# Optimization experiments

Hardware: AMD Instinct MI355X
Metric: run time of the kernel (lower is better)

The kernel has to match this reference:

```python
import jax, jax.numpy as jnp
from jax import lax
import numpy as np

LRELU_SLOPE = 0.01  # PyTorch LeakyReLU default
BETA = 0.25


def lrelu(x):
    return jnp.where(x >= 0, x, LRELU_SLOPE * x)


def conv2d(x, w, b, stride, pad):
    # x: [B,C,H,W], w: [Cout,Cin,k,k] (torch OIHW)
    y = lax.conv_general_dilated(x, w, (stride, stride), ((pad, pad), (pad, pad)),
                                 dimension_numbers=('NCHW', 'OIHW', 'NCHW'))
    return y + b[None, :, None, None]


def conv_transpose2d(x, w, b, stride, out_pad):
    # w: torch ConvTranspose2d weight [Cin,Cout,k,k]; implement as dilated conv
    # with spatially flipped kernel. out = (i-1)*stride + k + out_pad.
    wf = jnp.flip(w, (2, 3)).transpose(1, 0, 2, 3)  # -> [Cout,Cin,k,k]
    k = w.shape[2]
    pad = ((k - 1, k - 1 + out_pad), (k - 1, k - 1 + out_pad))
    y = lax.conv_general_dilated(x, wf, (1, 1), pad, lhs_dilation=(stride, stride),
                                 dimension_numbers=('NCHW', 'OIHW', 'NCHW'))
    return y + b[None, :, None, None]


def setup_inputs() -> dict:
    key = jax.random.key(0)
    ks = jax.random.split(key, 16)
    s = 0.05
    inp = {
        'x':   jax.random.normal(ks[0], (64, 1, 256, 256), jnp.float32),
        'ew1': jax.random.normal(ks[1], (8, 1, 4, 4), jnp.float32) * s,
        'eb1': jnp.zeros((8,), jnp.float32),
        'ew2': jax.random.normal(ks[2], (16, 8, 4, 4), jnp.float32) * s,
        'eb2': jnp.zeros((16,), jnp.float32),
        'ew3': jax.random.normal(ks[3], (32, 16, 4, 4), jnp.float32) * s,
        'eb3': jnp.zeros((32,), jnp.float32),
        'ew4': jax.random.normal(ks[4], (32, 32, 3, 3), jnp.float32) * s,
        'eb4': jnp.zeros((32,), jnp.float32),
        'ew5': jax.random.normal(ks[5], (64, 32, 1, 1), jnp.float32) * s,
        'eb5': jnp.zeros((64,), jnp.float32),
        'dw1': jax.random.normal(ks[6], (32, 64, 3, 3), jnp.float32) * s,
        'db1': jnp.zeros((32,), jnp.float32),
        'dw2': jax.random.normal(ks[7], (32, 16, 4, 4), jnp.float32) * s,
        'db2': jnp.zeros((16,), jnp.float32),
        'dw3': jax.random.normal(ks[8], (16, 8, 4, 4), jnp.float32) * s,
        'db3': jnp.zeros((8,), jnp.float32),
        'dw4': jax.random.normal(ks[9], (8, 1, 4, 4), jnp.float32) * s,
        'db4': jnp.zeros((1,), jnp.float32),
        # nn.init.uniform_(-1/K, 1/K) with K=512
        'codebook': jax.random.uniform(ks[10], (512, 64), jnp.float32,
                                       minval=-1.0 / 512, maxval=1.0 / 512),
    }
    return inp


def vqvae_forward(x, ew1, eb1, ew2, eb2, ew3, eb3, ew4, eb4, ew5, eb5,
                  dw1, db1, dw2, db2, dw3, db3, dw4, db4, codebook):
    # ---- encoder ----
    h = lrelu(conv2d(x, ew1, eb1, 2, 0))   # [B,8,127,127]
    h = lrelu(conv2d(h, ew2, eb2, 2, 0))   # [B,16,62,62]
    h = lrelu(conv2d(h, ew3, eb3, 2, 0))   # [B,32,30,30]
    h = lrelu(conv2d(h, ew4, eb4, 1, 1))   # [B,32,30,30]
    h = lrelu(conv2d(h, ew5, eb5, 1, 0))   # [B,64,30,30]
    # ---- vector quantizer ----
    lat = h.transpose(0, 2, 3, 1)                      # [B,h,w,D]
    D = lat.shape[-1]
    flat = lat.reshape(-1, D)                          # [N,D]
    # squared euclidean distances via expansion (same argmin as torch.norm)
    d2 = (jnp.sum(flat * flat, axis=1, keepdims=True)
          - 2.0 * flat @ codebook.T
          + jnp.sum(codebook * codebook, axis=1))      # [N,K]
    idx = jnp.argmin(d2, axis=1)                       # [N]
    q = codebook[idx].reshape(lat.shape)               # [B,h,w,D]
    commitment = jnp.mean((lax.stop_gradient(q) - lat) ** 2)
    embedding = jnp.mean((q - lax.stop_gradient(lat)) ** 2)
    vq_loss = commitment * BETA + embedding
    q_st = lat + lax.stop_gradient(q - lat)            # straight-through
    z = q_st.transpose(0, 3, 1, 2)                     # [B,D,h,w]
    # ---- decoder ----
    h = lrelu(conv2d(z, dw1, db1, 1, 1))               # [B,32,30,30]
    h = lrelu(conv_transpose2d(h, dw2, db2, 2, 1))     # [B,16,63,63]
    h = lrelu(conv_transpose2d(h, dw3, db3, 2, 1))     # [B,8,131,131]
    recons = jnp.tanh(conv_transpose2d(h, dw4, db4, 2, 0))  # [B,1,264,264]
    return recons, vq_loss


def reference(x, ew1, eb1, ew2, eb2, ew3, eb3, ew4, eb4, ew5, eb5,
              dw1, db1, dw2, db2, dw3, db3, dw4, db4, codebook):
    return vqvae_forward(x, ew1, eb1, ew2, eb2, ew3, eb3, ew4, eb4, ew5, eb5,
                         dw1, db1, dw2, db2, dw3, db3, dw4, db4, codebook)
```

## Files before the change

### kernel.cpp

```cpp
#include <hip/hip_runtime.h>
#include <hip/hip_bf16.h>
#include <math.h>

#define LRELU 0.01f

template<int NW>
__device__ __forceinline__ void ldw(const float* p, float* w) {
    if constexpr (NW % 4 == 0) {
#pragma unroll
        for (int u = 0; u < NW / 4; u++) {
            float4 v = *(const float4*)(p + 4 * u);
            w[4*u] = v.x; w[4*u+1] = v.y; w[4*u+2] = v.z; w[4*u+3] = v.w;
        }
    } else {
#pragma unroll
        for (int c = 0; c < NW; c++) w[c] = p[c];
    }
}

__device__ __forceinline__ void wfwd(const float* s, float* d, int CIN, int COUT,
                                     int KK, int i) {
    int co = i / (CIN * KK); int r = i - co * CIN * KK;
    int ci = r / KK; int t = r - ci * KK;
    d[(ci * KK + t) * COUT + co] = s[i];
}
__device__ __forceinline__ void wtr(const float* s, float* d, int CIN, int COUT,
                                    int KK, int i) {
    int ci = i / (COUT * KK); int r = i - ci * COUT * KK;
    int co = r / KK; int t = r - co * KK;
    d[(t * CIN + ci) * COUT + co] = s[i];
}
__global__ __launch_bounds__(256)
void prep_k(const float* e1, const float* e2, const float* e3, const float* e4,
            const float* e5, const float* d1, const float* d2, const float* d3,
            const float* d4, float* w, const float* cbp, float* hcbn,
            unsigned long long* keys, float* loss, int* idxm, int N) {
    int i = blockIdx.x * 256 + threadIdx.x;
    if      (i < 128)   wfwd(e1, w + 0,     1,  8, 16, i);
    else if (i < 2176)  wfwd(e2, w + 128,   8, 16, 16, i - 128);
    else if (i < 10368) wfwd(e3, w + 2176, 16, 32, 16, i - 2176);
    else if (i < 19584) wfwd(e4, w + 10368, 32, 32, 9, i - 10368);
    else if (i < 21632) wfwd(e5, w + 19584, 32, 64, 1, i - 19584);
    else if (i < 40064) wfwd(d1, w + 21632, 64, 32, 9, i - 21632);
    else if (i < 48256) wtr (d2, w + 40064, 32, 16, 16, i - 40064);
    else if (i < 50304) wtr (d3, w + 48256, 16,  8, 16, i - 48256);
    else if (i < 50432) wtr (d4, w + 50304,  8,  1, 16, i - 50304);
    else if (i < 50944) {
        int k = i - 50432;
        const float* c = cbp + k * 64;
        float s = 0.f;
#pragma unroll
        for (int d = 0; d < 64; d++) s = fmaf(c[d], c[d], s);
        hcbn[k] = 0.5f * s;
    } else if (i < 50944 + N) {
        keys[i - 50944] = 0xFFFFFFFFFFFFFFFFull;
    } else if (i == 50944 + N) {
        loss[0] = 0.f;
    } else if (i < 50945 + N + 64 * 124) {
        int j = i - (50945 + N);
        int b2 = j / 124, s = j - b2 * 124;
        int r, c;
        if (s < 32)      { r = 0;  c = s; }
        else if (s < 64) { r = 31; c = s - 32; }
        else { int u = s - 64; r = 1 + (u >> 1); c = (u & 1) * 31; }
        idxm[b2 * 1024 + r * 32 + c] = 512;
    }
}

__global__ __launch_bounds__(256)
void ubuild_k(const float* __restrict__ w, const float* __restrict__ cb,
              float* __restrict__ U) {
    int g = blockIdx.x * 256 + threadIdx.x;
    if (g >= 513 * 288) return;
    if (g >= 512 * 288) { U[g] = 0.f; return; }
    int k = g / 288, rem = g - k * 288;
    const float* cr = cb + k * 64;
    float s = 0.f;
#pragma unroll 4
    for (int ci = 0; ci < 64; ci++)
        s = fmaf(w[ci * 288 + rem], cr[ci], s);
    U[g] = s;
}

template<int CIN, int COUT, int CO_BLK, int HIN, int ISTR, int HOUT, int WOUT,
         int OPLANE, int OSTR, int OPAD, int CB, int RB, int ZCONV, int ZF_CH>
__global__ __launch_bounds__(256)
void convs2_k(const float* __restrict__ in, const float* __restrict__ wt,
              const float* __restrict__ bias, float* __restrict__ out) {
    const int b = blockIdx.x, cog = blockIdx.y, tid = threadIdx.x;
    if (ZF_CH > 0 && (int)blockIdx.z >= ZCONV) {
        if (cog != 0) return;
        int i = ((int)blockIdx.z - ZCONV) * 256 + tid;
        if (i >= ZF_CH * 124) return;
        int ch = i / 124, s = i - ch * 124;
        int r, c;
        if (s < 32)      { r = 0;  c = s; }
        else if (s < 64) { r = 31; c = s - 32; }
        else { int u = s - 64; r = 1 + (u >> 1); c = (u & 1) * 31; }
        out[(size_t)(b * ZF_CH + ch) * 1024 + r * 32 + c] = 0.f;
        return;
    }
    __shared__ __align__(16) float lw[CIN * 16 * CO_BLK];
    for (int i = tid; i < CIN * 16 * CO_BLK; i += 256) {
        int row = i / CO_BLK, c = i - row * CO_BLK;
        lw[i] = wt[row * COUT + cog * CO_BLK + c];
    }
    __syncthreads();

    const int tz = blockIdx.z;
    const int cbi = tz / RB, rb = tz - cbi * RB;
    const int tx = tid & 15, ty = tid >> 4;
    const int ow0 = (cbi * 16 + tx) * 2;
    const int oh  = rb * 16 + ty;
    if (oh >= HOUT || ow0 >= WOUT) return;
    const bool p1v = (ow0 + 1) < WOUT;

    float acc[CO_BLK][2];
#pragma unroll
    for (int c = 0; c < CO_BLK; c++) {
        float bv = bias[cog * CO_BLK + c];
        acc[c][0] = bv; acc[c][1] = bv;
    }
    const float* inb = in + ((size_t)(b * CIN) * HIN + oh * 2) * ISTR + ow0 * 2;
#pragma unroll 2
    for (int ci = 0; ci < CIN; ci++) {
        const float* r = inb + (size_t)ci * HIN * ISTR;
        float4 a4[4]; float2 b2[4];
#pragma unroll
        for (int kh = 0; kh < 4; kh++) {
            a4[kh] = *(const float4*)(r + kh * ISTR);
            b2[kh] = p1v ? *(const float2*)(r + kh * ISTR + 4) : make_float2(0.f, 0.f);
        }
        const float* wr = lw + ci * 16 * CO_BLK;
#pragma unroll
        for (int kh = 0; kh < 4; kh++) {
            float x0[4] = {a4[kh].x, a4[kh].y, a4[kh].z, a4[kh].w};
            float x1[4] = {a4[kh].z, a4[kh].w, b2[kh].x, b2[kh].y};
#pragma unroll
            for (int kw = 0; kw < 4; kw++) {
                float wv[CO_BLK];
                ldw<CO_BLK>(wr + (kh * 4 + kw) * CO_BLK, wv);
#pragma unroll
                for (int c = 0; c < CO_BLK; c++) {
                    acc[c][0] = fmaf(x0[kw], wv[c], acc[c][0]);
                    acc[c][1] = fmaf(x1[kw], wv[c], acc[c][1]);
                }
            }
        }
    }
    float* ob = out + (size_t)(b * COUT + cog * CO_BLK) * OPLANE
                    + (oh + OPAD) * OSTR + ow0 + OPAD;
#pragma unroll
    for (int c = 0; c < CO_BLK; c++) {
        float v0 = acc[c][0]; v0 = (v0 >= 0.f) ? v0 : LRELU * v0;
        ob[(size_t)c * OPLANE] = v0;
        if (p1v) {
            float v1 = acc[c][1]; v1 = (v1 >= 0.f) ? v1 : LRELU * v1;
            ob[(size_t)c * OPLANE + 1] = v1;
        }
    }
}

template<int CIN, int COUT, int CO_BLK, int OPLANE, int OSTR, int OPADH, int OPADV,
         bool ZSIDE>
__global__ __launch_bounds__(256)
void conv3_k(const float* __restrict__ in, const float* __restrict__ wt,
             const float* __restrict__ bias, float* __restrict__ out) {
    const int b = blockIdx.x, cog = blockIdx.y, tid = threadIdx.x;
    __shared__ __align__(16) float lw[CIN * 9 * CO_BLK];
    for (int i = tid; i < CIN * 9 * CO_BLK; i += 256) {
        int row = i / CO_BLK, c = i - row * CO_BLK;
        lw[i] = wt[row * COUT + cog * CO_BLK + c];
    }
    __syncthreads();

    const int rb = blockIdx.z;
    const int tx = tid & 15, ty = tid >> 4;
    const int r = rb * 16 + ty;
    if (r >= 30) return;
    const int ow0 = tx * 2;
    if (tx == 15) {
        if (ZSIDE) {
#pragma unroll
            for (int c = 0; c < CO_BLK; c++) {
                float* base = out + (size_t)(b * COUT + cog * CO_BLK + c) * OPLANE
                                  + (r + OPADV) * OSTR;
                base[0] = 0.f; base[31] = 0.f; base[32] = 0.f;
            }
        }
        return;
    }
    float acc[CO_BLK][2];
#pragma unroll
    for (int c = 0; c < CO_BLK; c++) {
        float bv = bias[cog * CO_BLK + c];
        acc[c][0] = bv; acc[c][1] = bv;
    }
    const float* inb = in + ((size_t)(b * CIN) * 32 + r) * 32 + ow0;
#pragma unroll 2
    for (int ci = 0; ci < CIN; ci++) {
        const float* rr = inb + (size_t)ci * 1024;
        float2 A[3], Bv[3];
#pragma unroll
        for (int kh = 0; kh < 3; kh++) {
            A[kh]  = *(const float2*)(rr + kh * 32);
            Bv[kh] = *(const float2*)(rr + kh * 32 + 2);
        }
        const float* wr = lw + ci * 9 * CO_BLK;
#pragma unroll
        for (int kh = 0; kh < 3; kh++) {
            float x0[3] = {A[kh].x, A[kh].y, Bv[kh].x};
            float x1[3] = {A[kh].y, Bv[kh].x, Bv[kh].y};
#pragma unroll
            for (int kw = 0; kw < 3; kw++) {
                float wv[CO_BLK];
                ldw<CO_BLK>(wr + (kh * 3 + kw) * CO_BLK, wv);
#pragma unroll
                for (int c = 0; c < CO_BLK; c++) {
                    acc[c][0] = fmaf(x0[kw], wv[c], acc[c][0]);
                    acc[c][1] = fmaf(x1[kw], wv[c], acc[c][1]);
                }
            }
        }
    }
    float* ob = out + (size_t)(b * COUT + cog * CO_BLK) * OPLANE
                    + (r + OPADV) * OSTR + ow0 + OPADH;
#pragma unroll
    for (int c = 0; c < CO_BLK; c++) {
        float v0 = acc[c][0]; v0 = (v0 >= 0.f) ? v0 : LRELU * v0;
        float v1 = acc[c][1]; v1 = (v1 >= 0.f) ? v1 : LRELU * v1;
        ob[(size_t)c * OPLANE] = v0;
        ob[(size_t)c * OPLANE + 1] = v1;
    }
}

template<int CIN, int COUT, int CO_BLK>
__global__ __launch_bounds__(256)
void conv1_k(const float* __restrict__ in, const float* __restrict__ wt,
             const float* __restrict__ bias, float* __restrict__ out) {
    __shared__ __align__(16) float lw[CIN * CO_BLK];
    const int b = blockIdx.x, cog = blockIdx.y;
    for (int i = threadIdx.x; i < CIN * CO_BLK; i += 256) {
        int row = i / CO_BLK, c = i - row * CO_BLK;
        lw[i] = wt[row * COUT + cog * CO_BLK + c];
    }
    __syncthreads();

    const int px4 = threadIdx.x * 4;
    float acc[CO_BLK][4];
#pragma unroll
    for (int c = 0; c < CO_BLK; c++) {
        float bv = bias[cog * CO_BLK + c];
        acc[c][0] = bv; acc[c][1] = bv; acc[c][2] = bv; acc[c][3] = bv;
    }
#pragma unroll 4
    for (int ci = 0; ci < CIN; ci++) {
        float4 x = *(const float4*)(in + (size_t)(b * CIN + ci) * 1024 + px4);
        float wv[CO_BLK];
        ldw<CO_BLK>(lw + ci * CO_BLK, wv);
#pragma unroll
        for (int c = 0; c < CO_BLK; c++) {
            acc[c][0] = fmaf(x.x, wv[c], acc[c][0]);
            acc[c][1] = fmaf(x.y, wv[c], acc[c][1]);
            acc[c][2] = fmaf(x.z, wv[c], acc[c][2]);
            acc[c][3] = fmaf(x.w, wv[c], acc[c][3]);
        }
    }
#pragma unroll
    for (int c = 0; c < CO_BLK; c++) {
        float4 v;
        v.x = (acc[c][0] >= 0.f) ? acc[c][0] : LRELU * acc[c][0];
        v.y = (acc[c][1] >= 0.f) ? acc[c][1] : LRELU * acc[c][1];
        v.z = (acc[c][2] >= 0.f) ? acc[c][2] : LRELU * acc[c][2];
        v.w = (acc[c][3] >= 0.f) ? acc[c][3] : LRELU * acc[c][3];
        *(float4*)(out + (size_t)(b * COUT + cog * CO_BLK + c) * 1024 + px4) = v;
    }
}

__global__ __launch_bounds__(256)
void d1tab_k(const int* __restrict__ idxm, const float* __restrict__ U,
             const float* __restrict__ bias, float* __restrict__ out) {
    const int b = blockIdx.x, cog = blockIdx.y, rt = blockIdx.z;
    const int tx = threadIdx.x & 31, ty = threadIdx.x >> 5;
    const int r = rt * 8 + ty;
    if (r >= 30) return;
    if (tx >= 30) {
        if (tx == 31) {
#pragma unroll
            for (int c = 0; c < 16; c++) {
                float* base = out + (size_t)(b * 32 + cog * 16 + c) * 1020 + r * 34;
                base[1] = 0.f; base[32] = 0.f; base[33] = 0.f;
            }
        }
        return;
    }
    const int* im = idxm + b * 1024 + r * 32 + tx;
    float acc[16];
#pragma unroll
    for (int c = 0; c < 16; c++) acc[c] = bias[cog * 16 + c];
#pragma unroll
    for (int kh = 0; kh < 3; kh++) {
        int i0 = im[kh * 32 + 0];
        int i1 = im[kh * 32 + 1];
        int i2 = im[kh * 32 + 2];
        const float4* u0 = (const float4*)(U + ((size_t)i0 * 9 + kh * 3 + 0) * 32 + cog * 16);
        const float4* u1 = (const float4*)(U + ((size_t)i1 * 9 + kh * 3 + 1) * 32 + cog * 16);
        const float4* u2 = (const float4*)(U + ((size_t)i2 * 9 + kh * 3 + 2) * 32 + cog * 16);
#pragma unroll
        for (int q = 0; q < 4; q++) {
            float4 a = u0[q], bb = u1[q], cc = u2[q];
            acc[4*q+0] += (a.x + bb.x) + cc.x;
            acc[4*q+1] += (a.y + bb.y) + cc.y;
            acc[4*q+2] += (a.z + bb.z) + cc.z;
            acc[4*q+3] += (a.w + bb.w) + cc.w;
        }
    }
    float* ob = out + (size_t)(b * 32 + cog * 16) * 1020 + r * 34 + tx + 2;
#pragma unroll
    for (int c = 0; c < 16; c++) {
        float v = acc[c]; v = (v >= 0.f) ? v : LRELU * v;
        ob[(size_t)c * 1020] = v;
    }
}

template<int CIN, int COUT, int CO_BLK, int HIN, int ISTR, int HOUT, int WOUT,
         int OPLANE, int OSTR, int OPADH, int NTX, int NT,
         int ZS_CH, int ZS_H, int ZS_STR, int ZC0, int ZC1, int ZC2,
         bool DO_TANH, bool DO_LOSS>
__global__ __launch_bounds__(256)
void convtf_k(const float* __restrict__ in, const float* __restrict__ wt,
              const float* __restrict__ bias, float* __restrict__ out,
              const float* __restrict__ loss, float* __restrict__ losstgt) {
    const int b = blockIdx.x, tid = threadIdx.x;
    const int NCOG = COUT / CO_BLK;
    int zz = blockIdx.z;
    if (zz >= NCOG * NT) {
        if (DO_LOSS) {
            if (b == 0 && tid == 0)
                losstgt[0] = 1.25f * loss[0] / (57600.f * 64.f);
            return;
        }
        int i = (zz - NCOG * NT) * 256 + tid;
        if (i >= ZS_CH * ZS_H * 3) return;
        int ch = i / (ZS_H * 3); int u = i - ch * ZS_H * 3;
        int r = u / 3, c3 = u - r * 3;
        int col = (c3 == 0) ? ZC0 : (c3 == 1) ? ZC1 : ZC2;
        out[((size_t)(b * ZS_CH + ch) * ZS_H + r) * ZS_STR + col] = 0.f;
        return;
    }
    const int cog = zz / NT, tile = zz - cog * NT;
    const int tlx = tile % NTX, tly = tile / NTX;

    __shared__ __align__(16) float lw[16 * CIN * CO_BLK];
    for (int i = tid; i < 16 * CIN * CO_BLK; i += 256) {
        int aq = i / (CIN * 4 * CO_BLK);
        int r1 = i - aq * (CIN * 4 * CO_BLK);
        int ci = r1 / (4 * CO_BLK);
        int u  = r1 - ci * (4 * CO_BLK);
        int pp = u / CO_BLK, c = u - pp * CO_BLK;
        int a = aq >> 1, q = aq & 1, py = pp >> 1, px = pp & 1;
        int tap = (py + 2 * a) * 4 + px + 2 * q;
        lw[i] = wt[((size_t)tap * CIN + ci) * COUT + cog * CO_BLK + c];
    }
    __syncthreads();

    const int SX = (WOUT + 1) >> 1, SY = (HOUT + 1) >> 1;
    const int sx0 = tlx * 32 + (tid & 15);
    const int sx1 = sx0 + 16;
    const int sy  = tly * 16 + (tid >> 4);
    const bool v0 = sx0 < SX, v1 = sx1 < SX;
    if (sy >= SY || !(v0 || v1)) return;

    const bool rvA = (sy < HIN);
    const bool rvB = (sy >= 1) && (sy <= HIN);

    float acc[2][4][CO_BLK];
#pragma unroll
    for (int s = 0; s < 2; s++)
#pragma unroll
        for (int o = 0; o < 4; o++)
#pragma unroll
            for (int c = 0; c < CO_BLK; c++)
                acc[s][o][c] = bias[cog * CO_BLK + c];

    const float* base = in + (size_t)(b * CIN) * HIN * ISTR;
#pragma unroll 2
    for (int ci = 0; ci < CIN; ci++) {
        const float* rowA = base + (size_t)ci * HIN * ISTR + (size_t)sy * ISTR;
        const float* rowB = rowA - ISTR;
        float rA0x = 0.f, rA0y = 0.f, rA1x = 0.f, rA1y = 0.f;
        float rB0x = 0.f, rB0y = 0.f, rB1x = 0.f, rB1y = 0.f;
        if (rvA) {
            if (v0) { rA0x = rowA[sx0]; rA0y = rowA[sx0 + 1]; }
            if (v1) { rA1x = rowA[sx1]; rA1y = rowA[sx1 + 1]; }
        }
        if (rvB) {
            if (v0) { rB0x = rowB[sx0]; rB0y = rowB[sx0 + 1]; }
            if (v1) { rB1x = rowB[sx1]; rB1y = rowB[sx1 + 1]; }
        }
#pragma unroll
        for (int a = 0; a < 2; a++) {
#pragma unroll
            for (int q = 0; q < 2; q++) {
                float iv0 = q ? (a ? rB0x : rA0x) : (a ? rB0y : rA0y);
                float iv1 = q ? (a ? rB1x : rA1x) : (a ? rB1y : rA1y);
                const float* wp = lw + (size_t)((a * 2 + q) * CIN + ci) * (4 * CO_BLK);
                float wv[4 * CO_BLK];
                ldw<4 * CO_BLK>(wp, wv);
#pragma unroll
                for (int o = 0; o < 4; o++)
#pragma unroll
                    for (int c = 0; c < CO_BLK; c++) {
                        acc[0][o][c] = fmaf(iv0, wv[o * CO_BLK + c], acc[0][o][c]);
                        acc[1][o][c] = fmaf(iv1, wv[o * CO_BLK + c], acc[1][o][c]);
                    }
            }
        }
    }
#pragma unroll
    for (int s = 0; s < 2; s++) {
        if (s ? !v1 : !v0) continue;
        const int sxx = s ? sx1 : sx0;
        const int ow = 2 * sxx;
        const bool full = (ow + 1) < WOUT;
#pragma unroll
        for (int py = 0; py < 2; py++) {
            int oh = 2 * sy + py;
            if (oh >= HOUT) continue;
            float* ob = out + (size_t)(b * COUT + cog * CO_BLK) * OPLANE
                            + (size_t)oh * OSTR + ow + OPADH;
#pragma unroll
            for (int c = 0; c < CO_BLK; c++) {
                float va = acc[s][py * 2 + 0][c];
                float vb = acc[s][py * 2 + 1][c];
                if (DO_TANH) { va = tanhf(va); vb = tanhf(vb); }
                else {
                    va = (va >= 0.f) ? va : LRELU * va;
                    vb = (vb >= 0.f) ? vb : LRELU * vb;
                }
                if ((OPADH & 1) == 0 && full) {
                    *(float2*)(ob + (size_t)c * OPLANE) = make_float2(va, vb);
                } else {
                    ob[(size_t)c * OPLANE] = va;
                    if (full) ob[(size_t)c * OPLANE + 1] = vb;
                }
            }
        }
    }
}

__global__ __launch_bounds__(256)
void vq_argmin_k(const float* __restrict__ lat, const float* __restrict__ cb,
                 const float* __restrict__ hcbn,
                 unsigned long long* __restrict__ keys) {
    const int pb = blockIdx.x;
    if (pb >= 225) return;
    __shared__ float4 scb4[1024];
    __shared__ float  shn[64];
    const int tid = threadIdx.x;
    const int dq  = tid & 3;
    const int pg  = tid >> 2;
    const int kbase = blockIdx.y * 64;
    const int posbase = pb * 256;

    const float4* src = (const float4*)(cb + (size_t)kbase * 64);
#pragma unroll
    for (int i = 0; i < 4; i++) scb4[tid + 256 * i] = src[tid + 256 * i];
    if (tid < 64) shn[tid] = hcbn[kbase + tid];

    float l[4][16];
    int   pidx[4];
#pragma unroll
    for (int j = 0; j < 4; j++) {
        int pos = posbase + pg + 64 * j;
        pidx[j] = pos;
        int b = pos / 900, p = pos - b * 900;
        int oh = p / 30, ow = p - oh * 30;
        int pp = 33 + oh * 32 + ow;
        const float* lb = lat + ((size_t)b * 64 + dq * 16) * 1024 + pp;
#pragma unroll
        for (int i = 0; i < 16; i++) l[j][i] = lb[i * 1024];
    }
    __syncthreads();

    float best[4] = {3.4e38f, 3.4e38f, 3.4e38f, 3.4e38f};
    int   bi[4]   = {0, 0, 0, 0};
#pragma unroll 2
    for (int k0 = 0; k0 < 64; k0++) {
        float4 c0 = scb4[k0 * 16 + dq * 4 + 0];
        float4 c1 = scb4[k0 * 16 + dq * 4 + 1];
        float4 c2 = scb4[k0 * 16 + dq * 4 + 2];
        float4 c3 = scb4[k0 * 16 + dq * 4 + 3];
        float hn = shn[k0];
#pragma unroll
        for (int j = 0; j < 4; j++) {
            float dot = 0.f;
            dot = fmaf(l[j][0],  c0.x, dot); dot = fmaf(l[j][1],  c0.y, dot);
            dot = fmaf(l[j][2],  c0.z, dot); dot = fmaf(l[j][3],  c0.w, dot);
            dot = fmaf(l[j][4],  c1.x, dot); dot = fmaf(l[j][5],  c1.y, dot);
            dot = fmaf(l[j][6],  c1.z, dot); dot = fmaf(l[j][7],  c1.w, dot);
            dot = fmaf(l[j][8],  c2.x, dot); dot = fmaf(l[j][9],  c2.y, dot);
            dot = fmaf(l[j][10], c2.z, dot); dot = fmaf(l[j][11], c2.w, dot);
            dot = fmaf(l[j][12], c3.x, dot); dot = fmaf(l[j][13], c3.y, dot);
            dot = fmaf(l[j][14], c3.z, dot); dot = fmaf(l[j][15], c3.w, dot);
            float full = dot + __shfl_xor(dot, 1);
            full += __shfl_xor(full, 2);
            float score = hn - full;
            if (score < best[j]) { best[j] = score; bi[j] = kbase + k0; }
        }
    }
    if (dq == 0) {
#pragma unroll
        for (int j = 0; j < 4; j++) {
            unsigned u = __float_as_uint(best[j]);
            u = ((int)u < 0) ? ~u : (u | 0x80000000u);
            unsigned long long key = ((unsigned long long)u << 32) | (unsigned)bi[j];
            atomicMin(&keys[pidx[j]], key);
        }
    }
}

__global__ __launch_bounds__(256)
void vq_finalize_k(const float* __restrict__ lat, const float* __restrict__ cb,
                   const unsigned long long* __restrict__ keys,
                   int* __restrict__ idxm, float* __restrict__ loss_acc, int B) {
    int gid = blockIdx.x * 256 + threadIdx.x;
    const int N = B * 900;
    float myloss = 0.f;
    if (gid < N) {
        int b = gid / 900, p = gid - b * 900;
        int oh = p / 30, ow = p - oh * 30;
        int pp = 33 + oh * 32 + ow;
        int idx = (int)(unsigned)(keys[gid] & 0xFFFFFFFFull);
        idxm[b * 1024 + pp] = idx;
        const float4* crow = (const float4*)(cb + (size_t)idx * 64);
        const float* lrow = lat + (size_t)b * 64 * 1024 + pp;
#pragma unroll
        for (int i = 0; i < 16; i++) {
            float4 cv = crow[i];
            float lv0 = lrow[(4 * i + 0) * 1024];
            float lv1 = lrow[(4 * i + 1) * 1024];
            float lv2 = lrow[(4 * i + 2) * 1024];
            float lv3 = lrow[(4 * i + 3) * 1024];
            float d0 = cv.x - lv0, d1 = cv.y - lv1, d2 = cv.z - lv2, d3 = cv.w - lv3;
            myloss = fmaf(d0, d0, myloss);
            myloss = fmaf(d1, d1, myloss);
            myloss = fmaf(d2, d2, myloss);
            myloss = fmaf(d3, d3, myloss);
        }
    }
    __shared__ float red[256];
    red[threadIdx.x] = myloss;
    __syncthreads();
    for (int s = 128; s > 0; s >>= 1) {
        if ((int)threadIdx.x < s) red[threadIdx.x] += red[threadIdx.x + s];
        __syncthreads();
    }
    if (threadIdx.x == 0) atomicAdd(loss_acc, red[0]);
}

static inline int nblk(long long total) { return (int)((total + 255) / 256); }

extern "C" void kernel_launch(void* const* d_in, const int* in_sizes, int n_in,
                              void* d_out, int out_size, void* d_ws, size_t ws_size,
                              hipStream_t stream) {
    const float* x   = (const float*)d_in[0];
    const float* ew1 = (const float*)d_in[1];  const float* eb1 = (const float*)d_in[2];
    const float* ew2 = (const float*)d_in[3];  const float* eb2 = (const float*)d_in[4];
    const float* ew3 = (const float*)d_in[5];  const float* eb3 = (const float*)d_in[6];
    const float* ew4 = (const float*)d_in[7];  const float* eb4 = (const float*)d_in[8];
    const float* ew5 = (const float*)d_in[9];  const float* eb5 = (const float*)d_in[10];
    const float* dw1 = (const float*)d_in[11]; const float* db1 = (const float*)d_in[12];
    const float* dw2 = (const float*)d_in[13]; const float* db2 = (const float*)d_in[14];
    const float* dw3 = (const float*)d_in[15]; const float* db3 = (const float*)d_in[16];
    const float* dw4 = (const float*)d_in[17]; const float* db4 = (const float*)d_in[18];
    const float* cb  = (const float*)d_in[19];
    float* out = (float*)d_out;

    const int B = in_sizes[0] / (256 * 256);
    const int N = B * 900;

    char* ws = (char*)d_ws;
    float* A     = (float*)(ws);
    float* Bb    = (float*)(ws + 34873344);
    float* d2out = (float*)(ws + 34873344);
    float* d3out = (float*)(ws);
    unsigned long long* keys = (unsigned long long*)(ws + 51126272);
    float* hcbn  = (float*)(ws + 51587072);
    int*   idxm  = (int*)(ws + 51589120);
    float* loss  = (float*)(ws + 52420608);
    float* wtb   = (float*)(ws + 52420864);
    float* U     = (float*)(ws + 52622592);
    float* ew1t = wtb;          float* ew2t = wtb + 128;
    float* ew3t = wtb + 2176;   float* ew4t = wtb + 10368;
    float* ew5t = wtb + 19584;  float* dw1t = wtb + 21632;
    float* dw2t = wtb + 40064;  float* dw3t = wtb + 48256;
    float* dw4t = wtb + 50304;

    prep_k<<<nblk(50945 + N + 64 * 124), 256, 0, stream>>>(
        ew1, ew2, ew3, ew4, ew5, dw1, dw2, dw3, dw4, wtb,
        cb, hcbn, keys, loss, idxm, N);
    ubuild_k<<<nblk(513 * 288), 256, 0, stream>>>(dw1t, cb, U);

    convs2_k<1, 8, 8, 256, 256, 127, 127, 127 * 128, 128, 0, 4, 8, 32, 0>
        <<<dim3(B, 1, 32), 256, 0, stream>>>(x, ew1t, eb1, A);
    convs2_k<8, 16, 4, 127, 128, 62, 62, 62 * 64, 64, 0, 2, 4, 8, 0>
        <<<dim3(B, 4, 8), 256, 0, stream>>>(A, ew2t, eb2, Bb);
    convs2_k<16, 32, 4, 62, 64, 30, 30, 1024, 32, 1, 1, 2, 2, 32>
        <<<dim3(B, 8, 18), 256, 0, stream>>>(Bb, ew3t, eb3, A);
    conv3_k<32, 32, 4, 1024, 32, 1, 1, false>
        <<<dim3(B, 8, 2), 256, 0, stream>>>(A, ew4t, eb4, Bb);
    conv1_k<32, 64, 4><<<dim3(B, 16, 1), 256, 0, stream>>>(Bb, ew5t, eb5, A);

    vq_argmin_k<<<dim3(232, 8), 256, 0, stream>>>(A, cb, hcbn, keys);
    vq_finalize_k<<<nblk(N), 256, 0, stream>>>(A, cb, keys, idxm, loss, B);

    d1tab_k<<<dim3(B, 2, 4), 256, 0, stream>>>(idxm, U, db1, A);
    convtf_k<32, 16, 4, 30, 34, 63, 63, 63 * 68, 68, 2, 1, 2,
             16, 63, 68, 1, 65, 66, false, false>
        <<<dim3(B, 1, 20), 256, 0, stream>>>(A + 1, dw2t, db2, d2out,
                                             nullptr, nullptr);
    convtf_k<16, 8, 8, 63, 68, 129, 129, 129 * 132, 132, 2, 3, 15,
             8, 129, 132, 1, 1, 131, false, false>
        <<<dim3(B, 1, 28), 256, 0, stream>>>(d2out + 1, dw3t, db3, d3out,
                                             nullptr, nullptr);
    convtf_k<8, 1, 1, 129, 132, 260, 260, 67600, 260, 0, 5, 45,
             0, 1, 1, 0, 0, 0, true, true>
        <<<dim3(B, 1, 46), 256, 0, stream>>>(d3out + 1, dw4t, db4, out, loss,
                                             out + (out_size - 1));
}
```

Before: 413.1 us.

## Restructure VQ argmin to one thread per position with uniform codebook loads

The VQ argmin kernel now gives each thread one full 64-dim latent vector in registers instead of splitting dimensions across four lanes with shuffle reductions. Codebook rows are read straight from global memory with wave-uniform addresses (likely scalar or broadcast loads) instead of being staged in shared memory, and each block covers 128 codes instead of 64, halving the grid's y dimension. This removes the cross-lane shuffles, the LDS staging and the barrier, and halves the atomicMin traffic, at the cost of much higher register pressure (64 latent floats per thread) and less parallelism per position.

```diff
diff --git a/kernel.cpp b/kernel.cpp
--- a/kernel.cpp
+++ b/kernel.cpp
@@ -455,69 +455,44 @@
                  unsigned long long* __restrict__ keys) {
     const int pb = blockIdx.x;
     if (pb >= 225) return;
-    __shared__ float4 scb4[1024];
-    __shared__ float  shn[64];
-    const int tid = threadIdx.x;
-    const int dq  = tid & 3;
-    const int pg  = tid >> 2;
-    const int kbase = blockIdx.y * 64;
-    const int posbase = pb * 256;
-
-    const float4* src = (const float4*)(cb + (size_t)kbase * 64);
-#pragma unroll
-    for (int i = 0; i < 4; i++) scb4[tid + 256 * i] = src[tid + 256 * i];
-    if (tid < 64) shn[tid] = hcbn[kbase + tid];
-
-    float l[4][16];
-    int   pidx[4];
-#pragma unroll
-    for (int j = 0; j < 4; j++) {
-        int pos = posbase + pg + 64 * j;
-        pidx[j] = pos;
-        int b = pos / 900, p = pos - b * 900;
-        int oh = p / 30, ow = p - oh * 30;
-        int pp = 33 + oh * 32 + ow;
-        const float* lb = lat + ((size_t)b * 64 + dq * 16) * 1024 + pp;
-#pragma unroll
-        for (int i = 0; i < 16; i++) l[j][i] = lb[i * 1024];
-    }
-    __syncthreads();
-
-    float best[4] = {3.4e38f, 3.4e38f, 3.4e38f, 3.4e38f};
-    int   bi[4]   = {0, 0, 0, 0};
-#pragma unroll 2
-    for (int k0 = 0; k0 < 64; k0++) {
-        float4 c0 = scb4[k0 * 16 + dq * 4 + 0];
-        float4 c1 = scb4[k0 * 16 + dq * 4 + 1];
-        float4 c2 = scb4[k0 * 16 + dq * 4 + 2];
-        float4 c3 = scb4[k0 * 16 + dq * 4 + 3];
-        float hn = shn[k0];
-#pragma unroll
-        for (int j = 0; j < 4; j++) {
-            float dot = 0.f;
-            dot = fmaf(l[j][0],  c0.x, dot); dot = fmaf(l[j][1],  c0.y, dot);
-            dot = fmaf(l[j][2],  c0.z, dot); dot = fmaf(l[j][3],  c0.w, dot);
-            dot = fmaf(l[j][4],  c1.x, dot); dot = fmaf(l[j][5],  c1.y, dot);
-            dot = fmaf(l[j][6],  c1.z, dot); dot = fmaf(l[j][7],  c1.w, dot);
-            dot = fmaf(l[j][8],  c2.x, dot); dot = fmaf(l[j][9],  c2.y, dot);
-            dot = fmaf(l[j][10], c2.z, dot); dot = fmaf(l[j][11], c2.w, dot);
-            dot = fmaf(l[j][12], c3.x, dot); dot = fmaf(l[j][13], c3.y, dot);
-            dot = fmaf(l[j][14], c3.z, dot); dot = fmaf(l[j][15], c3.w, dot);
-            float full = dot + __shfl_xor(dot, 1);
-            full += __shfl_xor(full, 2);
-            float score = hn - full;
-            if (score < best[j]) { best[j] = score; bi[j] = kbase + k0; }
-        }
-    }
-    if (dq == 0) {
-#pragma unroll
-        for (int j = 0; j < 4; j++) {
-            unsigned u = __float_as_uint(best[j]);
-            u = ((int)u < 0) ? ~u : (u | 0x80000000u);
-            unsigned long long key = ((unsigned long long)u << 32) | (unsigned)bi[j];
-            atomicMin(&keys[pidx[j]], key);
-        }
-    }
+    const int pos = pb * 256 + threadIdx.x;
+    const int kbase = blockIdx.y * 128;
+
+    int b = pos / 900, p = pos - b * 900;
+    int oh = p / 30, ow = p - oh * 30;
+    int pp = 33 + oh * 32 + ow;
+    const float* lb = lat + (size_t)b * 64 * 1024 + pp;
+    float l[64];
+#pragma unroll
+    for (int d = 0; d < 64; d++) l[d] = lb[(size_t)d * 1024];
+
+    float best = 3.4e38f;
+    int   bi   = 0;
+#pragma unroll 1
+    for (int k = 0; k < 128; k++) {
+        const float4* cp = (const float4*)(cb + (size_t)(kbase + k) * 64);
+        float hn = hcbn[kbase + k];
+        float a0 = 0.f, a1 = 0.f, a2 = 0.f, a3 = 0.f;
+#pragma unroll
+        for (int u = 0; u < 8; u++) {
+            float4 c0 = cp[2 * u];
+            float4 c1 = cp[2 * u + 1];
+            a0 = fmaf(l[8*u+0], c0.x, a0);
+            a1 = fmaf(l[8*u+1], c0.y, a1);
+            a2 = fmaf(l[8*u+2], c0.z, a2);
+            a3 = fmaf(l[8*u+3], c0.w, a3);
+            a0 = fmaf(l[8*u+4], c1.x, a0);
+            a1 = fmaf(l[8*u+5], c1.y, a1);
+            a2 = fmaf(l[8*u+6], c1.z, a2);
+            a3 = fmaf(l[8*u+7], c1.w, a3);
+        }
+        float score = hn - ((a0 + a1) + (a2 + a3));
+        if (score < best) { best = score; bi = kbase + k; }
+    }
+    unsigned u = __float_as_uint(best);
+    u = ((int)u < 0) ? ~u : (u | 0x80000000u);
+    unsigned long long key = ((unsigned long long)u << 32) | (unsigned)bi;
+    atomicMin(&keys[pos], key);
 }
 
 __global__ __launch_bounds__(256)
@@ -612,7 +587,7 @@
         <<<dim3(B, 8, 2), 256, 0, stream>>>(A, ew4t, eb4, Bb);
     conv1_k<32, 64, 4><<<dim3(B, 16, 1), 256, 0, stream>>>(Bb, ew5t, eb5, A);
 
-    vq_argmin_k<<<dim3(232, 8), 256, 0, stream>>>(A, cb, hcbn, keys);
+    vq_argmin_k<<<dim3(232, 4), 256, 0, stream>>>(A, cb, hcbn, keys);
     vq_finalize_k<<<nblk(N), 256, 0, stream>>>(A, cb, keys, idxm, loss, B);
 
     d1tab_k<<<dim3(B, 2, 4), 256, 0, stream>>>(idxm, U, db1, A);
```

Result: no change. 412.7 us (-0.1%).
